# Kernel tuning notes

Measured on AMD Instinct MI355X. Metric: run time of the kernel, lower is better.

## Reference

```python
import jax, jax.numpy as jnp
import numpy as np

N = 100_000   # nodes
E = 1_600_000 # edges (avg degree 16)
D = 64        # embed/hidden dim
V = 50_000    # vocab
G = 128       # graphs in batch
C = 20        # classes


def setup_inputs() -> dict:
    key = jax.random.key(0)
    ks = jax.random.split(key, 11)
    tokens = jax.random.randint(ks[0], (N,), 0, V)
    edge_src = jax.random.randint(ks[1], (E,), 0, N)
    edge_dst = jax.random.randint(ks[2], (E,), 0, N)
    graph_ids = jnp.sort(jax.random.randint(ks[3], (N,), 0, G))
    s = 1.0 / np.sqrt(D)
    return {
        "tokens": tokens,
        "edge_src": edge_src,
        "edge_dst": edge_dst,
        "graph_ids": graph_ids,
        "emb_table": jax.random.normal(ks[4], (V, D), jnp.float32) * 0.02,
        "W1": jax.random.normal(ks[5], (D, D), jnp.float32) * s,
        "b1": jax.random.normal(ks[6], (D,), jnp.float32) * s,
        "W2": jax.random.normal(ks[7], (D, D), jnp.float32) * s,
        "b2": jax.random.normal(ks[8], (D,), jnp.float32) * s,
        "Wc": jax.random.normal(ks[9], (D, C), jnp.float32) * s,
        "bc": jax.random.normal(ks[10], (C,), jnp.float32) * s,
    }


def reference(tokens, edge_src, edge_dst, graph_ids, emb_table, W1, b1, W2, b2, Wc, bc):
    # Embedding lookup: [N, D]
    h = emb_table[tokens]
    # in-degree per dst node (zero-degree nodes get 0 features, like DGL mean)
    deg = jax.ops.segment_sum(jnp.ones((E,), h.dtype), edge_dst, num_segments=N)
    inv_deg = (1.0 / jnp.maximum(deg, 1.0))[:, None]  # [N,1]

    def gcn(h, W, b):
        # copy_src + mean: gather src feats, segment-sum into dst, divide by degree
        agg = jax.ops.segment_sum(h[edge_src], edge_dst, num_segments=N) * inv_deg
        return jax.nn.relu(agg @ W + b)

    h = gcn(h, W1, b1)
    h = gcn(h, W2, b2)

    # dgl.mean_nodes: per-graph mean pooling
    cnt = jax.ops.segment_sum(jnp.ones((N,), h.dtype), graph_ids, num_segments=G)
    hg = jax.ops.segment_sum(h, graph_ids, num_segments=G) / jnp.maximum(cnt, 1.0)[:, None]
    return hg @ Wc + bc  # [G, C] logits
```

## Files before the change

kernel.cpp:

```cpp
#include <hip/hip_runtime.h>

#define DIM 64
#define CLS 20
#define SCAN_T 256
#define SCAN_E 1024
#define NBANDS 8
#define BBLOCKS 1024

__global__ void banded_count_kernel(const int* __restrict__ edst, int* __restrict__ deg,
                                    int N, int E) {
    int band   = blockIdx.x & (NBANDS - 1);
    int chunk  = blockIdx.x >> 3;
    int nchunk = gridDim.x >> 3;
    int bandSize = (N + NBANDS - 1) / NBANDS;
    int lo = band * bandSize;
    int hi = min(lo + bandSize, N);
    int per  = (E + nchunk - 1) / nchunk;
    int ebeg = chunk * per;
    int eend = min(ebeg + per, E);
    for (int e = ebeg + threadIdx.x; e < eend; e += blockDim.x) {
        int d = __builtin_nontemporal_load(&edst[e]);
        if (d >= lo && d < hi) atomicAdd(&deg[d], 1);
    }
}

__global__ void banded_scatter_kernel(const int* __restrict__ esrc, const int* __restrict__ edst,
                                      int* __restrict__ cursor, int* __restrict__ csr_src,
                                      int N, int E) {
    int band   = blockIdx.x & (NBANDS - 1);
    int chunk  = blockIdx.x >> 3;
    int nchunk = gridDim.x >> 3;
    int bandSize = (N + NBANDS - 1) / NBANDS;
    int lo = band * bandSize;
    int hi = min(lo + bandSize, N);
    int per  = (E + nchunk - 1) / nchunk;
    int ebeg = chunk * per;
    int eend = min(ebeg + per, E);
    for (int e = ebeg + threadIdx.x; e < eend; e += blockDim.x) {
        int d = __builtin_nontemporal_load(&edst[e]);
        int s = __builtin_nontemporal_load(&esrc[e]);
        if (d >= lo && d < hi) {
            int pos = atomicAdd(&cursor[d], 1);
            csr_src[pos] = s;
        }
    }
}

__global__ void scan1_kernel(const int* __restrict__ deg, int* __restrict__ rp,
                             int* __restrict__ bsum, int N) {
    __shared__ int sh[SCAN_T];
    int base = blockIdx.x * SCAN_E + threadIdx.x * 4;
    int v0 = (base + 0 < N) ? deg[base + 0] : 0;
    int v1 = (base + 1 < N) ? deg[base + 1] : 0;
    int v2 = (base + 2 < N) ? deg[base + 2] : 0;
    int v3 = (base + 3 < N) ? deg[base + 3] : 0;
    sh[threadIdx.x] = v0 + v1 + v2 + v3;
    __syncthreads();
    for (int off = 1; off < SCAN_T; off <<= 1) {
        int t = (threadIdx.x >= off) ? sh[threadIdx.x - off] : 0;
        __syncthreads();
        sh[threadIdx.x] += t;
        __syncthreads();
    }
    int run = (threadIdx.x > 0) ? sh[threadIdx.x - 1] : 0;
    if (base + 0 < N) rp[base + 0] = run; run += v0;
    if (base + 1 < N) rp[base + 1] = run; run += v1;
    if (base + 2 < N) rp[base + 2] = run; run += v2;
    if (base + 3 < N) rp[base + 3] = run;
    if (threadIdx.x == SCAN_T - 1) bsum[blockIdx.x] = sh[SCAN_T - 1];
}

__global__ void scan2_kernel(int* __restrict__ bsum, int NB) {
    __shared__ int sh[128];
    int v = (threadIdx.x < NB) ? bsum[threadIdx.x] : 0;
    sh[threadIdx.x] = v;
    __syncthreads();
    for (int off = 1; off < 128; off <<= 1) {
        int t = (threadIdx.x >= off) ? sh[threadIdx.x - off] : 0;
        __syncthreads();
        sh[threadIdx.x] += t;
        __syncthreads();
    }
    if (threadIdx.x < NB) bsum[threadIdx.x] = sh[threadIdx.x] - v;
}

__global__ void scan3_kernel(int* __restrict__ rp, int* __restrict__ cursor,
                             const int* __restrict__ bsum, int N) {
    int i = blockIdx.x * blockDim.x + threadIdx.x;
    if (i < N) {
        int v = rp[i] + bsum[i >> 10];
        rp[i] = v;
        cursor[i] = v;
    }
}

__global__ void embed_kernel(const int* __restrict__ tokens, const float* __restrict__ emb,
                             float* __restrict__ h, int N) {
    int t = blockIdx.x * blockDim.x + threadIdx.x;
    int n = t >> 4, c = t & 15;
    if (n < N) {
        int tok = tokens[n];
        ((float4*)h)[(size_t)n * 16 + c] = ((const float4*)emb)[(size_t)tok * 16 + c];
    }
}

__global__ void agg_csr_kernel(const int* __restrict__ rp, const int* __restrict__ deg,
                               const int* __restrict__ csr_src, const float* __restrict__ h,
                               float* __restrict__ agg, int N) {
    int n = (blockIdx.x * blockDim.x + threadIdx.x) >> 6;
    if (n >= N) return;
    int lane = threadIdx.x & 63;
    int j = lane >> 4, c = lane & 15;
    int beg = rp[n], d = deg[n];
    float ax = 0.f, ay = 0.f, az = 0.f, aw = 0.f;
    for (int e = j; e < d; e += 4) {
        int s = csr_src[beg + e];
        float4 v = ((const float4*)h)[(size_t)s * 16 + c];
        ax += v.x; ay += v.y; az += v.z; aw += v.w;
    }
    ax += __shfl_xor(ax, 16, 64); ay += __shfl_xor(ay, 16, 64);
    az += __shfl_xor(az, 16, 64); aw += __shfl_xor(aw, 16, 64);
    ax += __shfl_xor(ax, 32, 64); ay += __shfl_xor(ay, 32, 64);
    az += __shfl_xor(az, 32, 64); aw += __shfl_xor(aw, 32, 64);
    if (j == 0) {
        float4 o = {ax, ay, az, aw};
        ((float4*)agg)[(size_t)n * 16 + c] = o;
    }
}

__global__ void gemm_relu_kernel(const float* __restrict__ agg, const int* __restrict__ deg,
                                 const float* __restrict__ W, const float* __restrict__ b,
                                 float* __restrict__ out, int N) {
    __shared__ float4 Ws[64 * 16];
    __shared__ float4 bs[16];
    for (int i = threadIdx.x; i < 64 * 16; i += blockDim.x) Ws[i] = ((const float4*)W)[i];
    if (threadIdx.x < 16) bs[threadIdx.x] = ((const float4*)b)[threadIdx.x];
    __syncthreads();
    int n = blockIdx.x * blockDim.x + threadIdx.x;
    if (n >= N) return;
    float inv = 1.0f / fmaxf((float)deg[n], 1.0f);
    float4 hv[16];
    #pragma unroll
    for (int j = 0; j < 16; ++j) hv[j] = ((const float4*)agg)[(size_t)n * 16 + j];
    float4 acc[16];
    #pragma unroll
    for (int j = 0; j < 16; ++j) { acc[j].x = 0.f; acc[j].y = 0.f; acc[j].z = 0.f; acc[j].w = 0.f; }
    #pragma unroll
    for (int k4 = 0; k4 < 16; ++k4) {
        float4 hq = hv[k4];
        #pragma unroll
        for (int kk = 0; kk < 4; ++kk) {
            float hk = (kk == 0) ? hq.x : (kk == 1) ? hq.y : (kk == 2) ? hq.z : hq.w;
            int k = k4 * 4 + kk;
            #pragma unroll
            for (int j = 0; j < 16; ++j) {
                float4 w = Ws[k * 16 + j];
                acc[j].x = fmaf(hk, w.x, acc[j].x);
                acc[j].y = fmaf(hk, w.y, acc[j].y);
                acc[j].z = fmaf(hk, w.z, acc[j].z);
                acc[j].w = fmaf(hk, w.w, acc[j].w);
            }
        }
    }
    #pragma unroll
    for (int j = 0; j < 16; ++j) {
        float4 bb = bs[j];
        float4 o;
        o.x = fmaxf(fmaf(inv, acc[j].x, bb.x), 0.f);
        o.y = fmaxf(fmaf(inv, acc[j].y, bb.y), 0.f);
        o.z = fmaxf(fmaf(inv, acc[j].z, bb.z), 0.f);
        o.w = fmaxf(fmaf(inv, acc[j].w, bb.w), 0.f);
        ((float4*)out)[(size_t)n * 16 + j] = o;
    }
}

__device__ __forceinline__ int lower_bound_i(const int* a, int n, int key) {
    int lo = 0, hi = n;
    while (lo < hi) {
        int mid = (lo + hi) >> 1;
        if (a[mid] < key) lo = mid + 1; else hi = mid;
    }
    return lo;
}

__global__ void pool_head_kernel(const float* __restrict__ h, const int* __restrict__ gids,
                                 const float* __restrict__ Wc, const float* __restrict__ bc,
                                 float* __restrict__ out, int N) {
    __shared__ float4 red[256];
    __shared__ float hg[64];
    int g = blockIdx.x;
    int lo = lower_bound_i(gids, N, g);
    int hi = lower_bound_i(gids, N, g + 1);
    int r = threadIdx.x >> 4, c = threadIdx.x & 15;
    float ax = 0.f, ay = 0.f, az = 0.f, aw = 0.f;
    for (int n = lo + r; n < hi; n += 16) {
        float4 v = ((const float4*)h)[(size_t)n * 16 + c];
        ax += v.x; ay += v.y; az += v.z; aw += v.w;
    }
    float4 a = {ax, ay, az, aw};
    red[threadIdx.x] = a;
    __syncthreads();
    for (int s = 8; s > 0; s >>= 1) {
        if (r < s) {
            float4 m = red[r * 16 + c];
            float4 o = red[(r + s) * 16 + c];
            m.x += o.x; m.y += o.y; m.z += o.z; m.w += o.w;
            red[r * 16 + c] = m;
        }
        __syncthreads();
    }
    if (r == 0) {
        float icnt = 1.0f / fmaxf((float)(hi - lo), 1.0f);
        float4 m = red[c];
        hg[c * 4 + 0] = m.x * icnt;
        hg[c * 4 + 1] = m.y * icnt;
        hg[c * 4 + 2] = m.z * icnt;
        hg[c * 4 + 3] = m.w * icnt;
    }
    __syncthreads();
    if (threadIdx.x < CLS) {
        float s = bc[threadIdx.x];
        #pragma unroll
        for (int k = 0; k < 64; ++k) s = fmaf(hg[k], Wc[k * CLS + threadIdx.x], s);
        out[(size_t)g * CLS + threadIdx.x] = s;
    }
}

extern "C" void kernel_launch(void* const* d_in, const int* in_sizes, int n_in,
                              void* d_out, int out_size, void* d_ws, size_t ws_size,
                              hipStream_t stream) {
    const int*   tokens = (const int*)d_in[0];
    const int*   esrc   = (const int*)d_in[1];
    const int*   edst   = (const int*)d_in[2];
    const int*   gids   = (const int*)d_in[3];
    const float* emb    = (const float*)d_in[4];
    const float* W1     = (const float*)d_in[5];
    const float* b1     = (const float*)d_in[6];
    const float* W2     = (const float*)d_in[7];
    const float* b2     = (const float*)d_in[8];
    const float* Wc     = (const float*)d_in[9];
    const float* bc     = (const float*)d_in[10];
    int N = in_sizes[0];
    int E = in_sizes[1];
    float* out = (float*)d_out;

    float* h      = (float*)d_ws;
    float* agg    = h + (size_t)N * 64;
    int*   deg    = (int*)(agg + (size_t)N * 64);
    int*   rp     = deg + N;
    int*   cursor = rp + N;
    int*   csr    = cursor + N;
    int*   bsum   = csr + E;

    int NB = (N + SCAN_E - 1) / SCAN_E;

    hipMemsetAsync(deg, 0, (size_t)N * sizeof(int), stream);

    banded_count_kernel<<<BBLOCKS, 256, 0, stream>>>(edst, deg, N, E);
    scan1_kernel<<<NB, SCAN_T, 0, stream>>>(deg, rp, bsum, N);
    scan2_kernel<<<1, 128, 0, stream>>>(bsum, NB);
    scan3_kernel<<<(N + 255) / 256, 256, 0, stream>>>(rp, cursor, bsum, N);
    banded_scatter_kernel<<<BBLOCKS, 256, 0, stream>>>(esrc, edst, cursor, csr, N, E);

    embed_kernel<<<(N * 16 + 255) / 256, 256, 0, stream>>>(tokens, emb, h, N);

    agg_csr_kernel<<<((size_t)N * 64 + 255) / 256, 256, 0, stream>>>(rp, deg, csr, h, agg, N);
    gemm_relu_kernel<<<(N + 255) / 256, 256, 0, stream>>>(agg, deg, W1, b1, h, N);

    agg_csr_kernel<<<((size_t)N * 64 + 255) / 256, 256, 0, stream>>>(rp, deg, csr, h, agg, N);
    gemm_relu_kernel<<<(N + 255) / 256, 256, 0, stream>>>(agg, deg, W2, b2, h, N);

    pool_head_kernel<<<128, 256, 0, stream>>>(h, gids, Wc, bc, out, N);
}
```

Baseline: 464.7 us.

## Pre-partition edges into per-band queues before CSR count and scatter

Adds a partition pass that buckets (src,dst) edge pairs into 8 destination bands, using a shared-memory histogram and one global atomic reservation per band per block. The count and scatter kernels then read only their own band's queue instead of each band re-reading the full edge list and filtering. This removes the 8x redundant reads of edst/esrc, at the cost of one extra pass that writes and reads an int2 queue stored in the agg buffer. The queue depends on fixed per-band capacity QCAP=300000, which assumes roughly uniform destination distribution.

Measured after the change: 463.3 us. About the same (-0.3%).

```diff
diff --git a/kernel.cpp b/kernel.cpp
--- a/kernel.cpp
+++ b/kernel.cpp
@@ -6,43 +6,72 @@
 #define SCAN_E 1024
 #define NBANDS 8
 #define BBLOCKS 1024
-
-__global__ void banded_count_kernel(const int* __restrict__ edst, int* __restrict__ deg,
-                                    int N, int E) {
+#define CHUNK 2048
+#define QCAP 300000
+
+__global__ void init_qcur_kernel(int* __restrict__ qcur) {
+    if (threadIdx.x < NBANDS) qcur[threadIdx.x] = threadIdx.x * QCAP;
+}
+
+__global__ void partition_kernel(const int* __restrict__ esrc, const int* __restrict__ edst,
+                                 int2* __restrict__ queue, int* __restrict__ qcur,
+                                 int N, int E) {
+    __shared__ int hist[NBANDS];
+    __shared__ int pc[NBANDS];
+    int cbeg = blockIdx.x * CHUNK;
+    int cend = min(cbeg + CHUNK, E);
+    if (threadIdx.x < NBANDS) hist[threadIdx.x] = 0;
+    __syncthreads();
+    int bandSize = (N + NBANDS - 1) / NBANDS;
+    for (int e = cbeg + threadIdx.x; e < cend; e += blockDim.x) {
+        int d = edst[e];
+        atomicAdd(&hist[d / bandSize], 1);
+    }
+    __syncthreads();
+    if (threadIdx.x < NBANDS)
+        pc[threadIdx.x] = atomicAdd(&qcur[threadIdx.x], hist[threadIdx.x]);
+    __syncthreads();
+    for (int e = cbeg + threadIdx.x; e < cend; e += blockDim.x) {
+        int d = edst[e];
+        int s = esrc[e];
+        int b = d / bandSize;
+        int pos = atomicAdd(&pc[b], 1);
+        queue[pos] = make_int2(s, d);
+    }
+}
+
+__global__ void band_count_kernel(const int2* __restrict__ queue, const int* __restrict__ qcur,
+                                  int* __restrict__ deg) {
     int band   = blockIdx.x & (NBANDS - 1);
     int chunk  = blockIdx.x >> 3;
     int nchunk = gridDim.x >> 3;
-    int bandSize = (N + NBANDS - 1) / NBANDS;
-    int lo = band * bandSize;
-    int hi = min(lo + bandSize, N);
-    int per  = (E + nchunk - 1) / nchunk;
-    int ebeg = chunk * per;
-    int eend = min(ebeg + per, E);
-    for (int e = ebeg + threadIdx.x; e < eend; e += blockDim.x) {
-        int d = __builtin_nontemporal_load(&edst[e]);
-        if (d >= lo && d < hi) atomicAdd(&deg[d], 1);
-    }
-}
-
-__global__ void banded_scatter_kernel(const int* __restrict__ esrc, const int* __restrict__ edst,
-                                      int* __restrict__ cursor, int* __restrict__ csr_src,
-                                      int N, int E) {
+    int qbeg = band * QCAP;
+    int qend = qcur[band];
+    int len  = qend - qbeg;
+    int per  = (len + nchunk - 1) / nchunk;
+    int beg  = qbeg + chunk * per;
+    int end  = min(beg + per, qend);
+    for (int i = beg + threadIdx.x; i < end; i += blockDim.x) {
+        int2 e = queue[i];
+        atomicAdd(&deg[e.y], 1);
+    }
+}
+
+__global__ void band_scatter_kernel(const int2* __restrict__ queue, const int* __restrict__ qcur,
+                                    int* __restrict__ cursor, int* __restrict__ csr_src) {
     int band   = blockIdx.x & (NBANDS - 1);
     int chunk  = blockIdx.x >> 3;
     int nchunk = gridDim.x >> 3;
-    int bandSize = (N + NBANDS - 1) / NBANDS;
-    int lo = band * bandSize;
-    int hi = min(lo + bandSize, N);
-    int per  = (E + nchunk - 1) / nchunk;
-    int ebeg = chunk * per;
-    int eend = min(ebeg + per, E);
-    for (int e = ebeg + threadIdx.x; e < eend; e += blockDim.x) {
-        int d = __builtin_nontemporal_load(&edst[e]);
-        int s = __builtin_nontemporal_load(&esrc[e]);
-        if (d >= lo && d < hi) {
-            int pos = atomicAdd(&cursor[d], 1);
-            csr_src[pos] = s;
-        }
+    int qbeg = band * QCAP;
+    int qend = qcur[band];
+    int len  = qend - qbeg;
+    int per  = (len + nchunk - 1) / nchunk;
+    int beg  = qbeg + chunk * per;
+    int end  = min(beg + per, qend);
+    for (int i = beg + threadIdx.x; i < end; i += blockDim.x) {
+        int2 e = queue[i];
+        int pos = atomicAdd(&cursor[e.y], 1);
+        csr_src[pos] = e.x;
     }
 }
 
@@ -246,21 +275,25 @@
 
     float* h      = (float*)d_ws;
     float* agg    = h + (size_t)N * 64;
+    int2*  queue  = (int2*)agg;
     int*   deg    = (int*)(agg + (size_t)N * 64);
     int*   rp     = deg + N;
     int*   cursor = rp + N;
     int*   csr    = cursor + N;
     int*   bsum   = csr + E;
+    int*   qcur   = bsum + 128;
 
     int NB = (N + SCAN_E - 1) / SCAN_E;
 
     hipMemsetAsync(deg, 0, (size_t)N * sizeof(int), stream);
-
-    banded_count_kernel<<<BBLOCKS, 256, 0, stream>>>(edst, deg, N, E);
+    init_qcur_kernel<<<1, 64, 0, stream>>>(qcur);
+
+    partition_kernel<<<(E + CHUNK - 1) / CHUNK, 256, 0, stream>>>(esrc, edst, queue, qcur, N, E);
+    band_count_kernel<<<BBLOCKS, 256, 0, stream>>>(queue, qcur, deg);
     scan1_kernel<<<NB, SCAN_T, 0, stream>>>(deg, rp, bsum, N);
     scan2_kernel<<<1, 128, 0, stream>>>(bsum, NB);
     scan3_kernel<<<(N + 255) / 256, 256, 0, stream>>>(rp, cursor, bsum, N);
-    banded_scatter_kernel<<<BBLOCKS, 256, 0, stream>>>(esrc, edst, cursor, csr, N, E);
+    band_scatter_kernel<<<BBLOCKS, 256, 0, stream>>>(queue, qcur, cursor, csr);
 
     embed_kernel<<<(N * 16 + 255) / 256, 256, 0, stream>>>(tokens, emb, h, N);
 
```
